# Performance work log

Measured on AMD Instinct MI355X. Metric: run time of the kernel, lower is better.

The kernel has to match this reference:

```python
import jax, jax.numpy as jnp
import numpy as np

NEG_FILL = -1e9  # matches torch masked_fill(-1000000000.0)


def setup_inputs() -> dict:
    B, C, H, W = 32, 64, 256, 256
    HID = 128
    NZ = 8  # zone ids in [0, 8]
    key = jax.random.key(0)
    ks = jax.random.split(key, 8)
    pixel_logits = jax.random.normal(ks[0], (B, 1, H, W), dtype=jnp.float32)
    intermediate_features = jax.random.normal(ks[1], (B, C, H, W), dtype=jnp.float32)
    zone_patches = jax.random.randint(ks[2], (B, H, W), 0, NZ + 1, dtype=jnp.int32)
    cats = jax.random.randint(ks[3], (B,), 1, NZ + 1, dtype=jnp.int32)
    labels = jax.random.bernoulli(ks[4], 0.5, (B,)).astype(jnp.float32)
    W1 = jax.random.normal(ks[5], (HID, C), dtype=jnp.float32) * 0.05
    b1 = jnp.zeros((HID,), dtype=jnp.float32)
    W2 = jax.random.normal(ks[6], (HID,), dtype=jnp.float32) * 0.05
    b2 = jnp.zeros((), dtype=jnp.float32)
    return {
        "pixel_logits": pixel_logits,
        "intermediate_features": intermediate_features,
        "zone_patches": zone_patches,
        "cats": cats,
        "labels": labels,
        "W1": W1,
        "b1": b1,
        "W2": W2,
        "b2": b2,
    }


def reference(pixel_logits, intermediate_features, zone_patches, cats, labels, W1, b1, W2, b2):
    B, _, H, W = pixel_logits.shape
    # attention_net: 1x1 conv C->128, ReLU, 1x1 conv 128->1  (per-pixel MLP)
    h = jax.nn.relu(jnp.einsum('bchw,kc->bkhw', intermediate_features, W1)
                    + b1[None, :, None, None])            # (B,128,H,W)
    scores = jnp.einsum('bkhw,k->bhw', h, W2) + b2        # (B,H,W)

    mask = (zone_patches == cats[:, None, None]) & (zone_patches > 0)  # (B,H,W) bool
    maskf = mask.astype(scores.dtype)

    # scores * mask, then fill masked positions with -1e9 (exactly as torch code)
    att = jnp.where(mask, scores * maskf, NEG_FILL)
    weights = jax.nn.softmax(att.reshape(B, -1), axis=-1).reshape(B, H, W)

    has = maskf.sum(axis=(1, 2)) > 0                      # (B,) any valid slope pixels
    bag = jnp.sum(pixel_logits[:, 0] * weights * maskf, axis=(1, 2))
    bag = jnp.where(has, bag, 0.0)
    attention_maps = jnp.where(has[:, None, None], weights, 0.0)

    # BCEWithLogitsLoss (mean reduction), numerically stable
    x, y = bag, labels
    loss = jnp.mean(jnp.maximum(x, 0) - x * y + jnp.log1p(jnp.exp(-jnp.abs(x))))
    return loss, attention_maps
```

## Files before the change

### kernel.cpp

```cpp
#include <hip/hip_runtime.h>
#include <math.h>

#define HW       65536
#define NCH      64
#define HIDDEN   128
#define NBATCH   32
#define NPIX     (NBATCH * HW)
#define WIN      2048
#define NBLK     (NPIX / WIN)
#define WPB      (HW / WIN)
#define NEG_FILL -1e9f

__global__ __launch_bounds__(256, 2) void mask_mlp_kernel(
    const float* __restrict__ feat,
    const float* __restrict__ W1,
    const float* __restrict__ b1,
    const float* __restrict__ W2,
    const float* __restrict__ b2,
    const int*   __restrict__ zone,
    const int*   __restrict__ cats,
    float*       __restrict__ att,
    float*       __restrict__ pmax,
    float*       __restrict__ psum)
{
    __shared__ __align__(16) float sW[NCH][HIDDEN];
    __shared__ __align__(16) float sFc[NCH][64];
    __shared__ __align__(16) float sfull[WIN];
    __shared__ unsigned short slist[WIN];
    __shared__ float sred[8];
    __shared__ int lcnt;

    const int tid  = threadIdx.x;
    const int lane = tid & 63;
    const int wid  = tid >> 6;
    const int b    = blockIdx.x >> 5;
    const int win0 = (blockIdx.x & 31) * WIN;

    if (tid == 0) lcnt = 0;
    __syncthreads();

    #pragma unroll
    for (int r = 0; r < 8; ++r) {
        int idx = tid + r * 256;
        int k   = idx & 127;
        int c4  = idx >> 7;
        float4 v = *(const float4*)(W1 + k * NCH + c4 * 4);
        sW[c4 * 4 + 0][k] = v.x;
        sW[c4 * 4 + 1][k] = v.y;
        sW[c4 * 4 + 2][k] = v.z;
        sW[c4 * 4 + 3][k] = v.w;
    }

    {
        float4 nf = make_float4(NEG_FILL, NEG_FILL, NEG_FILL, NEG_FILL);
        *(float4*)&sfull[tid * 4]         = nf;
        *(float4*)&sfull[(tid + 256) * 4] = nf;
    }

    {
        const int  catb = cats[b];
        const int* zp   = zone + (size_t)b * HW + win0;
        #pragma unroll
        for (int j = 0; j < 8; ++j) {
            int  px = j * 256 + tid;
            int  z  = zp[px];
            bool m  = (z == catb) && (z > 0);
            unsigned long long bal = __ballot(m);
            int rank = __popcll(bal & ((1ull << lane) - 1ull));
            int base = 0;
            if (lane == 0) {
                int cnt = __popcll(bal);
                if (cnt) base = atomicAdd(&lcnt, cnt);
            }
            base = __shfl(base, 0, 64);
            if (m) slist[base + rank] = (unsigned short)px;
        }
    }
    __syncthreads();

    const int n  = lcnt;
    const int nt = (n + 63) >> 6;

    const int tx = tid & 15;
    const int ty = tid >> 4;

    float b1v[8], w2v[8];
    *(float4*)&b1v[0] = *(const float4*)(b1 + tx * 4);
    *(float4*)&b1v[4] = *(const float4*)(b1 + 64 + tx * 4);
    *(float4*)&w2v[0] = *(const float4*)(W2 + tx * 4);
    *(float4*)&w2v[4] = *(const float4*)(W2 + 64 + tx * 4);
    const float b2v = b2[0];

    const float* fb = feat + (size_t)b * NCH * HW + win0;

    for (int t = 0; t < nt; ++t) {
        {
            int  p     = tid & 63;
            int  cw    = tid >> 6;
            int  slot  = t * 64 + p;
            bool valid = slot < n;
            int  lpx   = valid ? (int)slist[slot] : 0;
            const float* fp = fb + lpx;
            #pragma unroll
            for (int cc = 0; cc < 16; ++cc) {
                int c = cw * 16 + cc;
                float v = 0.f;
                if (valid) v = fp[(size_t)c * HW];
                sFc[c][p] = v;
            }
        }
        __syncthreads();

        float acc[4][8];
        #pragma unroll
        for (int i = 0; i < 4; ++i)
            #pragma unroll
            for (int j = 0; j < 8; ++j) acc[i][j] = 0.f;

        #pragma unroll 8
        for (int c = 0; c < NCH; ++c) {
            float a[4], w[8];
            *(float4*)&a[0] = *(const float4*)&sFc[c][ty * 4];
            *(float4*)&w[0] = *(const float4*)&sW[c][tx * 4];
            *(float4*)&w[4] = *(const float4*)&sW[c][64 + tx * 4];
            #pragma unroll
            for (int i = 0; i < 4; ++i)
                #pragma unroll
                for (int j = 0; j < 8; ++j)
                    acc[i][j] = fmaf(a[i], w[j], acc[i][j]);
        }

        #pragma unroll
        for (int i = 0; i < 4; ++i) {
            float s = 0.f;
            #pragma unroll
            for (int j = 0; j < 8; ++j) {
                float h = acc[i][j] + b1v[j];
                h = h > 0.f ? h : 0.f;
                s = fmaf(w2v[j], h, s);
            }
            s += __shfl_xor(s, 1, 64);
            s += __shfl_xor(s, 2, 64);
            s += __shfl_xor(s, 4, 64);
            s += __shfl_xor(s, 8, 64);
            if (tx == 0) {
                int slot = t * 64 + ty * 4 + i;
                if (slot < n) sfull[slist[slot]] = s + b2v;
            }
        }
        __syncthreads();
    }

    float4 x0 = *(float4*)&sfull[tid * 8];
    float4 x1 = *(float4*)&sfull[tid * 8 + 4];
    float m = fmaxf(fmaxf(fmaxf(x0.x, x0.y), fmaxf(x0.z, x0.w)),
                    fmaxf(fmaxf(x1.x, x1.y), fmaxf(x1.z, x1.w)));
    #pragma unroll
    for (int k = 1; k < 64; k <<= 1) m = fmaxf(m, __shfl_xor(m, k, 64));
    if (lane == 0) sred[wid] = m;
    __syncthreads();
    const float M = fmaxf(fmaxf(sred[0], sred[1]), fmaxf(sred[2], sred[3]));

    float es = expf(x0.x - M) + expf(x0.y - M) + expf(x0.z - M) + expf(x0.w - M)
             + expf(x1.x - M) + expf(x1.y - M) + expf(x1.z - M) + expf(x1.w - M);
    #pragma unroll
    for (int k = 1; k < 64; k <<= 1) es += __shfl_xor(es, k, 64);
    if (lane == 0) sred[4 + wid] = es;
    __syncthreads();
    if (tid == 0) {
        pmax[blockIdx.x] = M;
        psum[blockIdx.x] = sred[4] + sred[5] + sred[6] + sred[7];
    }

    float* ap = att + (size_t)b * HW + win0;
    #pragma unroll
    for (int r = 0; r < 8; ++r)
        ap[r * 256 + tid] = sfull[r * 256 + tid];
}

__global__ __launch_bounds__(64) void merge_kernel(
    const float* __restrict__ pmax, const float* __restrict__ psum,
    float* __restrict__ maxv, float* __restrict__ sumv, float* __restrict__ bag)
{
    const int b = blockIdx.x;
    const int t = threadIdx.x;
    float m = -3.4e38f, s = 0.f;
    if (t < WPB) { m = pmax[b * WPB + t]; s = psum[b * WPB + t]; }
    float M = m;
    #pragma unroll
    for (int k = 1; k < 64; k <<= 1) M = fmaxf(M, __shfl_xor(M, k, 64));
    float z = s * expf(m - M);
    #pragma unroll
    for (int k = 1; k < 64; k <<= 1) z += __shfl_xor(z, k, 64);
    if (t == 0) { maxv[b] = M; sumv[b] = z; bag[b] = 0.f; }
}

__global__ __launch_bounds__(256) void finalize_kernel(
    float* __restrict__ att,
    const float* __restrict__ logits,
    const float* __restrict__ maxv, const float* __restrict__ sumv,
    float* __restrict__ bag)
{
    const int idx = blockIdx.x * 256 + threadIdx.x;
    const int b   = idx >> 16;
    const float mx  = maxv[b];
    const bool  has = mx > -5e8f;
    const float inv = 1.f / sumv[b];

    const float a = att[idx];
    const float w = has ? expf(a - mx) * inv : 0.f;
    att[idx] = w;

    float part = w * logits[idx];
    #pragma unroll
    for (int s = 1; s < 64; s <<= 1) part += __shfl_xor(part, s, 64);
    __shared__ float r[4];
    if ((threadIdx.x & 63) == 0) r[threadIdx.x >> 6] = part;
    __syncthreads();
    if (threadIdx.x == 0) atomicAdd(&bag[b], r[0] + r[1] + r[2] + r[3]);
}

__global__ __launch_bounds__(64) void loss_kernel(
    const float* __restrict__ bag, const float* __restrict__ labels,
    float* __restrict__ out)
{
    const int t = threadIdx.x;
    float l = 0.f;
    if (t < NBATCH) {
        float x = bag[t], y = labels[t];
        l = fmaxf(x, 0.f) - x * y + log1pf(expf(-fabsf(x)));
    }
    #pragma unroll
    for (int s = 1; s < 64; s <<= 1) l += __shfl_xor(l, s, 64);
    if (t == 0) out[0] = l * (1.f / NBATCH);
}

extern "C" void kernel_launch(void* const* d_in, const int* in_sizes, int n_in,
                              void* d_out, int out_size, void* d_ws, size_t ws_size,
                              hipStream_t stream)
{
    const float* logits = (const float*)d_in[0];
    const float* feat   = (const float*)d_in[1];
    const int*   zone   = (const int*)  d_in[2];
    const int*   cats   = (const int*)  d_in[3];
    const float* labels = (const float*)d_in[4];
    const float* W1     = (const float*)d_in[5];
    const float* b1v    = (const float*)d_in[6];
    const float* W2     = (const float*)d_in[7];
    const float* b2v    = (const float*)d_in[8];

    float* out = (float*)d_out;
    float* att = out + 1;

    float* wsf   = (float*)d_ws;
    float* pmaxb = wsf;
    float* psumb = wsf + NBLK;
    float* maxv  = wsf + 2 * NBLK;
    float* sumv  = maxv + NBATCH;
    float* bag   = sumv + NBATCH;

    mask_mlp_kernel<<<NBLK, 256, 0, stream>>>(feat, W1, b1v, W2, b2v, zone, cats,
                                              att, pmaxb, psumb);
    merge_kernel   <<<NBATCH, 64, 0, stream>>>(pmaxb, psumb, maxv, sumv, bag);
    finalize_kernel<<<NPIX / 256, 256, 0, stream>>>(att, logits, maxv, sumv, bag);
    loss_kernel    <<<1, 64, 0, stream>>>(bag, labels, out);
}
```

Measured before the change: 837.0 us.

## Stream masked scores directly to output with online softmax and fold merge into finalize

```diff
diff --git a/kernel.cpp b/kernel.cpp
--- a/kernel.cpp
+++ b/kernel.cpp
@@ -11,7 +11,7 @@
 #define WPB      (HW / WIN)
 #define NEG_FILL -1e9f
 
-__global__ __launch_bounds__(256, 2) void mask_mlp_kernel(
+__global__ __launch_bounds__(256, 3) void mask_mlp_kernel(
     const float* __restrict__ feat,
     const float* __restrict__ W1,
     const float* __restrict__ b1,
@@ -25,14 +25,12 @@
 {
     __shared__ __align__(16) float sW[NCH][HIDDEN];
     __shared__ __align__(16) float sFc[NCH][64];
-    __shared__ __align__(16) float sfull[WIN];
     __shared__ unsigned short slist[WIN];
     __shared__ float sred[8];
     __shared__ int lcnt;
 
     const int tid  = threadIdx.x;
     const int lane = tid & 63;
-    const int wid  = tid >> 6;
     const int b    = blockIdx.x >> 5;
     const int win0 = (blockIdx.x & 31) * WIN;
 
@@ -49,12 +47,6 @@
         sW[c4 * 4 + 1][k] = v.y;
         sW[c4 * 4 + 2][k] = v.z;
         sW[c4 * 4 + 3][k] = v.w;
-    }
-
-    {
-        float4 nf = make_float4(NEG_FILL, NEG_FILL, NEG_FILL, NEG_FILL);
-        *(float4*)&sfull[tid * 4]         = nf;
-        *(float4*)&sfull[(tid + 256) * 4] = nf;
     }
 
     {
@@ -92,6 +84,9 @@
     const float b2v = b2[0];
 
     const float* fb = feat + (size_t)b * NCH * HW + win0;
+    float*       ap = att  + (size_t)b * HW + win0;
+
+    float mrun = -3.4e38f, srun = 0.f;
 
     for (int t = 0; t < nt; ++t) {
         {
@@ -145,94 +140,125 @@
             s += __shfl_xor(s, 8, 64);
             if (tx == 0) {
                 int slot = t * 64 + ty * 4 + i;
-                if (slot < n) sfull[slist[slot]] = s + b2v;
+                if (slot < n) {
+                    float v = s + b2v;
+                    ap[slist[slot]] = v;
+                    float nm = fmaxf(mrun, v);
+                    srun = srun * expf(mrun - nm) + expf(v - nm);
+                    mrun = nm;
+                }
             }
         }
         __syncthreads();
     }
 
-    float4 x0 = *(float4*)&sfull[tid * 8];
-    float4 x1 = *(float4*)&sfull[tid * 8 + 4];
-    float m = fmaxf(fmaxf(fmaxf(x0.x, x0.y), fmaxf(x0.z, x0.w)),
-                    fmaxf(fmaxf(x1.x, x1.y), fmaxf(x1.z, x1.w)));
-    #pragma unroll
-    for (int k = 1; k < 64; k <<= 1) m = fmaxf(m, __shfl_xor(m, k, 64));
-    if (lane == 0) sred[wid] = m;
-    __syncthreads();
-    const float M = fmaxf(fmaxf(sred[0], sred[1]), fmaxf(sred[2], sred[3]));
-
-    float es = expf(x0.x - M) + expf(x0.y - M) + expf(x0.z - M) + expf(x0.w - M)
-             + expf(x1.x - M) + expf(x1.y - M) + expf(x1.z - M) + expf(x1.w - M);
-    #pragma unroll
-    for (int k = 1; k < 64; k <<= 1) es += __shfl_xor(es, k, 64);
-    if (lane == 0) sred[4 + wid] = es;
+    {
+        float m = mrun, s = srun;
+        #pragma unroll
+        for (int k = 1; k < 64; k <<= 1) {
+            float mo = __shfl_xor(m, k, 64);
+            float so = __shfl_xor(s, k, 64);
+            float nm = fmaxf(m, mo);
+            s = s * expf(m - nm) + so * expf(mo - nm);
+            m = nm;
+        }
+        if (lane == 0) { sred[tid >> 6] = m; sred[4 + (tid >> 6)] = s; }
+    }
     __syncthreads();
     if (tid == 0) {
+        float M = sred[0], S = sred[4];
+        #pragma unroll
+        for (int i = 1; i < 4; ++i) {
+            float mo = sred[i], so = sred[4 + i];
+            float nm = fmaxf(M, mo);
+            S = S * expf(M - nm) + so * expf(mo - nm);
+            M = nm;
+        }
         pmax[blockIdx.x] = M;
-        psum[blockIdx.x] = sred[4] + sred[5] + sred[6] + sred[7];
-    }
-
-    float* ap = att + (size_t)b * HW + win0;
-    #pragma unroll
-    for (int r = 0; r < 8; ++r)
-        ap[r * 256 + tid] = sfull[r * 256 + tid];
-}
-
-__global__ __launch_bounds__(64) void merge_kernel(
-    const float* __restrict__ pmax, const float* __restrict__ psum,
-    float* __restrict__ maxv, float* __restrict__ sumv, float* __restrict__ bag)
-{
-    const int b = blockIdx.x;
-    const int t = threadIdx.x;
-    float m = -3.4e38f, s = 0.f;
-    if (t < WPB) { m = pmax[b * WPB + t]; s = psum[b * WPB + t]; }
-    float M = m;
-    #pragma unroll
-    for (int k = 1; k < 64; k <<= 1) M = fmaxf(M, __shfl_xor(M, k, 64));
-    float z = s * expf(m - M);
-    #pragma unroll
-    for (int k = 1; k < 64; k <<= 1) z += __shfl_xor(z, k, 64);
-    if (t == 0) { maxv[b] = M; sumv[b] = z; bag[b] = 0.f; }
+        psum[blockIdx.x] = S;
+    }
 }
 
 __global__ __launch_bounds__(256) void finalize_kernel(
     float* __restrict__ att,
     const float* __restrict__ logits,
-    const float* __restrict__ maxv, const float* __restrict__ sumv,
-    float* __restrict__ bag)
-{
-    const int idx = blockIdx.x * 256 + threadIdx.x;
-    const int b   = idx >> 16;
-    const float mx  = maxv[b];
-    const bool  has = mx > -5e8f;
-    const float inv = 1.f / sumv[b];
+    const int*   __restrict__ zone,
+    const int*   __restrict__ cats,
+    const float* __restrict__ pmaxb, const float* __restrict__ psumb,
+    float* __restrict__ pbag)
+{
+    __shared__ float sM, sInv;
+    __shared__ int   sHas;
+    __shared__ float r4[4];
+
+    const int bid = blockIdx.x;
+    const int b   = bid >> 8;
+    const int tid = threadIdx.x;
+
+    if (tid < 64) {
+        float m = -3.4e38f, sv = 0.f;
+        if (tid < WPB) { m = pmaxb[b * WPB + tid]; sv = psumb[b * WPB + tid]; }
+        float M = m;
+        #pragma unroll
+        for (int k = 1; k < 64; k <<= 1) M = fmaxf(M, __shfl_xor(M, k, 64));
+        float z = sv * expf(m - M);
+        #pragma unroll
+        for (int k = 1; k < 64; k <<= 1) z += __shfl_xor(z, k, 64);
+        if (tid == 0) {
+            bool has = M > -5e8f;
+            sM   = M;
+            sHas = has ? 1 : 0;
+            sInv = has ? (1.f / z) : 0.f;
+        }
+    }
+    __syncthreads();
+
+    const float M   = sM;
+    const float inv = sInv;
+    const bool  has = sHas != 0;
+
+    const int idx  = bid * 256 + tid;
+    const int catb = cats[b];
+    const int z    = zone[idx];
+    const bool mk  = (z == catb) && (z > 0);
 
     const float a = att[idx];
-    const float w = has ? expf(a - mx) * inv : 0.f;
+    const float w = (mk && has) ? expf(a - M) * inv : 0.f;
     att[idx] = w;
 
     float part = w * logits[idx];
     #pragma unroll
     for (int s = 1; s < 64; s <<= 1) part += __shfl_xor(part, s, 64);
-    __shared__ float r[4];
-    if ((threadIdx.x & 63) == 0) r[threadIdx.x >> 6] = part;
-    __syncthreads();
-    if (threadIdx.x == 0) atomicAdd(&bag[b], r[0] + r[1] + r[2] + r[3]);
-}
-
-__global__ __launch_bounds__(64) void loss_kernel(
-    const float* __restrict__ bag, const float* __restrict__ labels,
+    if ((tid & 63) == 0) r4[tid >> 6] = part;
+    __syncthreads();
+    if (tid == 0) pbag[bid] = r4[0] + r4[1] + r4[2] + r4[3];
+}
+
+__global__ __launch_bounds__(1024) void loss_kernel(
+    const float* __restrict__ pbag, const float* __restrict__ labels,
     float* __restrict__ out)
 {
-    const int t = threadIdx.x;
-    float l = 0.f;
-    if (t < NBATCH) {
-        float x = bag[t], y = labels[t];
-        l = fmaxf(x, 0.f) - x * y + log1pf(expf(-fabsf(x)));
-    }
-    #pragma unroll
-    for (int s = 1; s < 64; s <<= 1) l += __shfl_xor(l, s, 64);
-    if (t == 0) out[0] = l * (1.f / NBATCH);
+    __shared__ float lred[32];
+    const int tid = threadIdx.x;
+    const int b   = tid >> 5;
+    const int j   = tid & 31;
+
+    float s = 0.f;
+    #pragma unroll
+    for (int r = 0; r < 8; ++r) s += pbag[b * 256 + j + r * 32];
+    #pragma unroll
+    for (int k = 1; k < 32; k <<= 1) s += __shfl_xor(s, k, 64);
+    if (j == 0) {
+        float x = s, y = labels[b];
+        lred[b] = fmaxf(x, 0.f) - x * y + log1pf(expf(-fabsf(x)));
+    }
+    __syncthreads();
+    if (tid < 64) {
+        float l = (tid < 32) ? lred[tid] : 0.f;
+        #pragma unroll
+        for (int k = 1; k < 64; k <<= 1) l += __shfl_xor(l, k, 64);
+        if (tid == 0) out[0] = l * (1.f / NBATCH);
+    }
 }
 
 extern "C" void kernel_launch(void* const* d_in, const int* in_sizes, int n_in,
@@ -255,13 +281,11 @@
     float* wsf   = (float*)d_ws;
     float* pmaxb = wsf;
     float* psumb = wsf + NBLK;
-    float* maxv  = wsf + 2 * NBLK;
-    float* sumv  = maxv + NBATCH;
-    float* bag   = sumv + NBATCH;
+    float* pbag  = wsf + 2 * NBLK;
 
     mask_mlp_kernel<<<NBLK, 256, 0, stream>>>(feat, W1, b1v, W2, b2v, zone, cats,
                                               att, pmaxb, psumb);
-    merge_kernel   <<<NBATCH, 64, 0, stream>>>(pmaxb, psumb, maxv, sumv, bag);
-    finalize_kernel<<<NPIX / 256, 256, 0, stream>>>(att, logits, maxv, sumv, bag);
-    loss_kernel    <<<1, 64, 0, stream>>>(bag, labels, out);
-}
+    finalize_kernel<<<NPIX / 256, 256, 0, stream>>>(att, logits, zone, cats,
+                                                    pmaxb, psumb, pbag);
+    loss_kernel    <<<1, 1024, 0, stream>>>(pbag, labels, out);
+}
```

New measurement: 780.5 us. -6.8%, faster.
